# Performance work log

Measured on AMD Instinct MI355X. Metric: run time of the kernel, lower is better.

Reference implementation:

```python
import jax, jax.numpy as jnp
import numpy as np
from jax import lax

# Module config (from init_kwargs)
PADDING = (1, 1)
DILATION = (1, 1)
GROUPS = 1
# stride param is initialized to ones(2); effective integer stride = floor(stride) = (1, 1).
# Output shape depends on this value, so it must be static under jit.
INT_STRIDE = (1, 1)


def setup_inputs() -> dict:
    key = jax.random.key(0)
    k1, k2 = jax.random.split(key)
    B, Cin, H, W = 32, 128, 64, 64
    Cout, kH, kW = 256, 3, 3
    x = jax.random.normal(k1, (B, Cin, H, W), dtype=jnp.float32)
    # reset_parameters: uniform(-stdv, stdv), stdv = 1/sqrt(Cin*kH*kW)
    stdv = 1.0 / np.sqrt(Cin * kH * kW)
    weight = jax.random.uniform(k2, (Cout, Cin // GROUPS, kH, kW), dtype=jnp.float32,
                                minval=-stdv, maxval=stdv)
    stride = jnp.ones((2,), dtype=jnp.float32)
    return {"x": x, "weight": weight, "stride": stride}


def reference(x, weight, stride):
    # Integer strides = floor(stride); with stride initialized to ones this is (1, 1).
    # (Static under jit; floor has zero derivative a.e., so stride only affects
    #  sampling locations, exactly as in the CUDA im2col forward.)
    out = lax.conv_general_dilated(
        x, weight,
        window_strides=INT_STRIDE,
        padding=[(PADDING[0], PADDING[0]), (PADDING[1], PADDING[1])],
        rhs_dilation=DILATION,
        dimension_numbers=("NCHW", "OIHW", "NCHW"),
        feature_group_count=GROUPS,
    )
    return out
```

## Files before the change

### kernel.cpp

```cpp
#include <hip/hip_runtime.h>

typedef __attribute__((ext_vector_type(8))) short short8;
typedef __attribute__((ext_vector_type(4))) float f32x4;

#define XP_ELEMS (32u * 66u * 66u * 128u)
#define WT_ELEMS (256u * 1152u)
#define WS_NEED  ((size_t)(XP_ELEMS + WT_ELEMS) * 2u)

typedef const __attribute__((address_space(1))) void* gp1_t;
typedef __attribute__((address_space(3))) void* lp3_t;

__device__ __forceinline__ void gload16(const void* g, void* l) {
  __builtin_amdgcn_global_load_lds((gp1_t)g, (lp3_t)l, 16, 0, 0);
}

__device__ __forceinline__ short f2bf(float f) {
  unsigned u = __float_as_uint(f);
  u = (u + 0x7FFFu + ((u >> 16) & 1u)) >> 16;
  return (short)u;
}

__global__ __launch_bounds__(256) void prepass_x(const float* __restrict__ x,
                                                 short* __restrict__ xp) {
  __shared__ short lds[64 * 128];
  const int y = blockIdx.x;
  const int b = blockIdx.y;
  const int t = threadIdx.x;

  const float* src = x + (long)b * 128 * 4096 + y * 64;
#pragma unroll
  for (int i = 0; i < 8; ++i) {
    int f4 = t + i * 256;
    int cin = f4 >> 4, px4 = f4 & 15;
    float4 v = *(const float4*)(src + (long)cin * 4096 + px4 * 4);
    float vv[4] = {v.x, v.y, v.z, v.w};
#pragma unroll
    for (int j = 0; j < 4; ++j) {
      int px = px4 * 4 + j;
      int g = (cin >> 3) ^ ((px ^ (px >> 2)) & 15);
      lds[px * 128 + (g << 3) + (cin & 7)] = f2bf(vv[j]);
    }
  }
  __syncthreads();
  short* dst = xp + ((long)(b * 66 + y + 1) * 66 + 1) * 128;
#pragma unroll
  for (int i = 0; i < 4; ++i) {
    int f8 = t + i * 256;
    int px = f8 >> 4, c8 = f8 & 15;
    int g = c8 ^ ((px ^ (px >> 2)) & 15);
    short8 v = *(const short8*)&lds[px * 128 + (g << 3)];
    *(short8*)(dst + (long)px * 128 + c8 * 8) = v;
  }
  short8 z = (short8)0;
  short* rowbase = xp + (long)(b * 66 + y + 1) * 66 * 128;
  if (t < 32) {
    int px = (t < 16) ? 0 : 65;
    int c8 = t & 15;
    *(short8*)(rowbase + (long)px * 128 + c8 * 8) = z;
  }
  if (y == 0) {
    short* r0 = xp + (long)(b * 66) * 66 * 128;
    for (int idx = t; idx < 66 * 16; idx += 256) *(short8*)(r0 + idx * 8) = z;
  }
  if (y == 63) {
    short* r65 = xp + ((long)(b * 66) + 65) * 66 * 128;
    for (int idx = t; idx < 66 * 16; idx += 256) *(short8*)(r65 + idx * 8) = z;
  }
}

__global__ __launch_bounds__(256) void prepass_w(const float* __restrict__ w,
                                                 short* __restrict__ wt) {
  int o    = blockIdx.x * 256 + threadIdx.x;
  int cout = o / 1152;
  int r    = o % 1152;
  int kh   = r / 384;
  int kw   = (r / 128) % 3;
  int cin  = r & 127;
  wt[o] = f2bf(w[((cout * 128 + cin) * 3 + kh) * 3 + kw]);
}

__global__ __launch_bounds__(512, 2) void conv_gemm(const short* __restrict__ xp,
                                                    const short* __restrict__ wt,
                                                    float* __restrict__ out) {
  __shared__ alignas(16) short Alds[2 * 2 * 2 * 128 * 32];
  __shared__ alignas(16) short Blds[2 * 2 * 2 * 128 * 32];
  const int tid = threadIdx.x;
  const int w   = tid >> 6;
  const int l   = tid & 63;
  const int l15 = l & 15;
  const int q   = l >> 4;
  const int wm2 = w >> 2;
  const int wn4 = w & 3;
  const int ntile = blockIdx.x;

  const int r6 = (tid >> 2) & 63;
  const int cc = tid >> 8;
  const int pp = tid & 3;
  const int cs = pp ^ ((r6 >> 1) & 3);
  const int aTh  = r6 * 1152 + cc * 32 + cs * 8;
  const int ldsA = cc * 4096 + r6 * 32 + pp * 8;
  const int ldsB0 = ldsA + ((r6 & 32) << 5);
  int bTh[2][2];
#pragma unroll
  for (int hb = 0; hb < 2; ++hb)
#pragma unroll
    for (int nq = 0; nq < 2; ++nq) {
      int R  = (r6 & 31) + ((r6 >> 5) << 6) + nq * 32;
      int n  = (ntile << 8) + (hb << 7) + R;
      int bb = n >> 12, yy = (n >> 6) & 63, xx = n & 63;
      bTh[hb][nq] = ((bb * 66 + yy) * 66 + xx) * 128 + cc * 32 + cs * 8;
    }

  int aRd[8], bRd[4];
#pragma unroll
  for (int mi = 0; mi < 8; ++mi) {
    int r = (mi << 4) + l15;
    aRd[mi] = r * 32 + ((q ^ ((r >> 1) & 3)) << 3);
  }
#pragma unroll
  for (int nj = 0; nj < 4; ++nj) {
    int r = ((wn4 & 1) << 6) + (nj << 4) + l15;
    bRd[nj] = r * 32 + ((q ^ ((r >> 1) & 3)) << 3);
  }
  const int aHB = wm2 * 8192;
  const int bHB = (wn4 >> 1) * 8192;

  f32x4 acc[8][4];
#pragma unroll
  for (int mi = 0; mi < 8; ++mi)
#pragma unroll
    for (int nj = 0; nj < 4; ++nj) acc[mi][nj] = (f32x4)0.f;

  short8 af[4][2], bf[4][2];

  auto ST_A = [&](int s, int v, int kb) {
    gload16(wt + kb + v * 73728 + aTh,
            &Alds[s * 16384 + v * 2048 + ldsA]);
    gload16(wt + kb + 147456 + v * 73728 + aTh,
            &Alds[s * 16384 + 8192 + v * 2048 + ldsA]);
  };
  auto ST_B = [&](int s, int nq, int sh) {
    gload16(xp + sh + bTh[0][nq], &Blds[s * 16384 + (nq << 10) + ldsB0]);
    gload16(xp + sh + bTh[1][nq], &Blds[s * 16384 + 8192 + (nq << 10) + ldsB0]);
  };
  auto LD_A = [&](int s, int mq) {
#pragma unroll
    for (int i = 0; i < 4; ++i)
#pragma unroll
      for (int c = 0; c < 2; ++c)
        af[i][c] = *(const short8*)&Alds[s * 16384 + aHB + c * 4096 + aRd[mq * 4 + i]];
  };
  auto LD_B = [&](int s, int nq) {
#pragma unroll
    for (int j = 0; j < 2; ++j)
#pragma unroll
      for (int c = 0; c < 2; ++c)
        bf[nq * 2 + j][c] =
            *(const short8*)&Blds[s * 16384 + bHB + c * 4096 + bRd[nq * 2 + j]];
  };
  auto MM = [&](int mq, int nq) {
    __builtin_amdgcn_s_setprio(1);
#pragma unroll
    for (int c = 0; c < 2; ++c)
#pragma unroll
      for (int i = 0; i < 4; ++i)
#pragma unroll
        for (int j = 0; j < 2; ++j)
          acc[mq * 4 + i][nq * 2 + j] = __builtin_amdgcn_mfma_f32_16x16x32_bf16(
              af[i][c], bf[nq * 2 + j][c], acc[mq * 4 + i][nq * 2 + j], 0, 0, 0);
    __builtin_amdgcn_s_setprio(0);
  };

#define BAR()   do { __builtin_amdgcn_s_barrier(); \
                     asm volatile("" ::: "memory"); } while (0)
#define LGKM0() asm volatile("s_waitcnt lgkmcnt(0)" ::: "memory")
#define VMC(n)  asm volatile("s_waitcnt vmcnt(" #n ")" ::: "memory")

  ST_A(0, 0, 0);  ST_B(0, 0, 0);
  ST_A(0, 1, 0);  ST_B(0, 1, 0);
  ST_A(1, 0, 64); ST_B(1, 0, 64);
  VMC(4);
  BAR();

#pragma unroll
  for (int J = 0; J < 9; ++J) {
    const int kh  = J / 3,        kw  = J % 3;
    const int khn = (J + 1) / 3,  kwn = (J + 1) % 3;
    const int kb1 = J * 128 + 64;
    const int kb2 = (J + 1) * 128;
    const int sh1 = (kh * 66 + kw) * 128 + 64;
    const int sh2 = (khn * 66 + kwn) * 128;
    const int sh3 = sh2 + 64;

    LD_A(0, 0); LD_B(0, 0);
    ST_A(1, 1, kb1);
    LGKM0(); MM(0, 0);
    LD_B(0, 1);
    ST_B(1, 1, sh1);
    LGKM0(); MM(0, 1);
    BAR();

    LD_A(0, 1);
    if (J < 8) ST_A(0, 0, kb2);
    LGKM0(); MM(1, 0);
    if (J < 8) ST_B(0, 0, sh2);
    LGKM0(); MM(1, 1);
    if (J < 8) { VMC(4); } else { VMC(0); }
    BAR();

    LD_A(1, 0); LD_B(1, 0);
    if (J < 8) ST_A(0, 1, kb2);
    LGKM0(); MM(0, 0);
    LD_B(1, 1);
    if (J < 8) ST_B(0, 1, sh2);
    LGKM0(); MM(0, 1);
    BAR();

    LD_A(1, 1);
    if (J < 8) ST_A(1, 0, kb2 + 64);
    LGKM0(); MM(1, 0);
    if (J < 8) ST_B(1, 0, sh3);
    LGKM0(); MM(1, 1);
    if (J < 8) { VMC(4); BAR(); }
  }

  const int bimg = ntile >> 4;
  const int yx0  = ((ntile & 15) << 8) + (wn4 << 6) + l15;
  float* outb = out + (long)bimg * (256 * 4096) + yx0;
#pragma unroll
  for (int mi = 0; mi < 8; ++mi) {
#pragma unroll
    for (int r = 0; r < 4; ++r) {
      const int cout = (wm2 << 7) + (mi << 4) + (q << 2) + r;
      float* orow = outb + (long)cout * 4096;
#pragma unroll
      for (int nj = 0; nj < 4; ++nj) orow[nj << 4] = acc[mi][nj][r];
    }
  }
#undef BAR
#undef LGKM0
#undef VMC
}

__global__ __launch_bounds__(256) void naive_conv(const float* __restrict__ x,
                                                  const float* __restrict__ wgt,
                                                  float* __restrict__ out) {
  long o = (long)blockIdx.x * 256 + threadIdx.x;
  int xx = (int)(o & 63);
  int y  = (int)((o >> 6) & 63);
  int co = (int)((o >> 12) & 255);
  int b  = (int)(o >> 20);
  float s = 0.f;
  for (int ci = 0; ci < 128; ++ci) {
    for (int kh = 0; kh < 3; ++kh) {
      int iy = y + kh - 1;
      if (iy < 0 || iy > 63) continue;
      for (int kw = 0; kw < 3; ++kw) {
        int ix = xx + kw - 1;
        if (ix < 0 || ix > 63) continue;
        s += x[((long)(b * 128 + ci) * 64 + iy) * 64 + ix] *
             wgt[((co * 128 + ci) * 3 + kh) * 3 + kw];
      }
    }
  }
  out[o] = s;
}

extern "C" void kernel_launch(void* const* d_in, const int* in_sizes, int n_in,
                              void* d_out, int out_size, void* d_ws, size_t ws_size,
                              hipStream_t stream) {
  (void)in_sizes; (void)n_in;
  const float* x   = (const float*)d_in[0];
  const float* wgt = (const float*)d_in[1];
  float* out = (float*)d_out;
  if (ws_size >= WS_NEED) {
    short* xp = (short*)d_ws;
    short* wt = xp + XP_ELEMS;
    prepass_x<<<dim3(64, 32), dim3(256), 0, stream>>>(x, xp);
    prepass_w<<<dim3(WT_ELEMS / 256), dim3(256), 0, stream>>>(wgt, wt);
    conv_gemm<<<dim3(512), dim3(512), 0, stream>>>(xp, wt, out);
  } else {
    naive_conv<<<dim3(out_size / 256), dim3(256), 0, stream>>>(x, wgt, out);
  }
}
```

Before: 254.2 us.

## Load weights directly from global into MFMA fragments with pre-swizzled layout

```diff
diff --git a/kernel.cpp b/kernel.cpp
--- a/kernel.cpp
+++ b/kernel.cpp
@@ -9,6 +9,7 @@
 
 typedef const __attribute__((address_space(1))) void* gp1_t;
 typedef __attribute__((address_space(3))) void* lp3_t;
+typedef const __attribute__((address_space(1))) short8* g8p_t;
 
 __device__ __forceinline__ void gload16(const void* g, void* l) {
   __builtin_amdgcn_global_load_lds((gp1_t)g, (lp3_t)l, 16, 0, 0);
@@ -76,14 +77,16 @@
   int kh   = r / 384;
   int kw   = (r / 128) % 3;
   int cin  = r & 127;
-  wt[o] = f2bf(w[((cout * 128 + cin) * 3 + kh) * 3 + kw]);
+  int mb = cout >> 4, l15 = cout & 15;
+  int c32 = r >> 5, q = (r >> 3) & 3, k7 = r & 7;
+  wt[((mb * 36 + c32) << 9) + (l15 << 5) + (q << 3) + k7] =
+      f2bf(w[((cout * 128 + cin) * 3 + kh) * 3 + kw]);
 }
 
 __global__ __launch_bounds__(512, 2) void conv_gemm(const short* __restrict__ xp,
                                                     const short* __restrict__ wt,
                                                     float* __restrict__ out) {
-  __shared__ alignas(16) short Alds[2 * 2 * 2 * 128 * 32];
-  __shared__ alignas(16) short Blds[2 * 2 * 2 * 128 * 32];
+  __shared__ alignas(16) short Blds[2 * 16384];
   const int tid = threadIdx.x;
   const int w   = tid >> 6;
   const int l   = tid & 63;
@@ -97,9 +100,7 @@
   const int cc = tid >> 8;
   const int pp = tid & 3;
   const int cs = pp ^ ((r6 >> 1) & 3);
-  const int aTh  = r6 * 1152 + cc * 32 + cs * 8;
-  const int ldsA = cc * 4096 + r6 * 32 + pp * 8;
-  const int ldsB0 = ldsA + ((r6 & 32) << 5);
+  const int ldsB0 = cc * 4096 + r6 * 32 + pp * 8 + ((r6 & 32) << 5);
   int bTh[2][2];
 #pragma unroll
   for (int hb = 0; hb < 2; ++hb)
@@ -111,46 +112,49 @@
       bTh[hb][nq] = ((bb * 66 + yy) * 66 + xx) * 128 + cc * 32 + cs * 8;
     }
 
-  int aRd[8], bRd[4];
-#pragma unroll
-  for (int mi = 0; mi < 8; ++mi) {
-    int r = (mi << 4) + l15;
-    aRd[mi] = r * 32 + ((q ^ ((r >> 1) & 3)) << 3);
-  }
+  int bRd[4];
 #pragma unroll
   for (int nj = 0; nj < 4; ++nj) {
     int r = ((wn4 & 1) << 6) + (nj << 4) + l15;
     bRd[nj] = r * 32 + ((q ^ ((r >> 1) & 3)) << 3);
   }
-  const int aHB = wm2 * 8192;
   const int bHB = (wn4 >> 1) * 8192;
 
+  const int aV = l15 * 32 + q * 8;
+
   f32x4 acc[8][4];
 #pragma unroll
   for (int mi = 0; mi < 8; ++mi)
 #pragma unroll
     for (int nj = 0; nj < 4; ++nj) acc[mi][nj] = (f32x4)0.f;
 
-  short8 af[4][2], bf[4][2];
-
-  auto ST_A = [&](int s, int v, int kb) {
-    gload16(wt + kb + v * 73728 + aTh,
-            &Alds[s * 16384 + v * 2048 + ldsA]);
-    gload16(wt + kb + 147456 + v * 73728 + aTh,
-            &Alds[s * 16384 + 8192 + v * 2048 + ldsA]);
+  short8 afA[4][2], afB[4][2], bf[4][2];
+
+#define BAR()   do { __builtin_amdgcn_s_barrier(); \
+                     asm volatile("" ::: "memory"); } while (0)
+#define LGK0()  asm volatile("s_waitcnt lgkmcnt(0)" ::: "memory")
+#define VMC(n)  asm volatile("s_waitcnt vmcnt(" #n ")" ::: "memory")
+
+  auto ALOAD = [&](int T, int mq, short8 (&d)[4][2]) {
+    const int mb0 = wm2 * 8 + mq * 4;
+#pragma unroll
+    for (int i = 0; i < 4; ++i)
+#pragma unroll
+      for (int c = 0; c < 2; ++c)
+        d[i][c] = *(g8p_t)(wt + (((long)((mb0 + i) * 36 + 2 * T + c) << 9) + aV));
   };
   auto ST_B = [&](int s, int nq, int sh) {
     gload16(xp + sh + bTh[0][nq], &Blds[s * 16384 + (nq << 10) + ldsB0]);
     gload16(xp + sh + bTh[1][nq], &Blds[s * 16384 + 8192 + (nq << 10) + ldsB0]);
   };
-  auto LD_A = [&](int s, int mq) {
-#pragma unroll
-    for (int i = 0; i < 4; ++i)
-#pragma unroll
-      for (int c = 0; c < 2; ++c)
-        af[i][c] = *(const short8*)&Alds[s * 16384 + aHB + c * 4096 + aRd[mq * 4 + i]];
-  };
-  auto LD_B = [&](int s, int nq) {
+  auto BSTAGE = [&](int T) {
+    const int J = T >> 1, h = T & 1;
+    const int kh = J / 3, kw = J - kh * 3;
+    const int sh = (kh * 66 + kw) * 128 + h * 64;
+    ST_B(T & 1, 0, sh);
+    ST_B(T & 1, 1, sh);
+  };
+  auto BREAD = [&](int s, int nq) {
 #pragma unroll
     for (int j = 0; j < 2; ++j)
 #pragma unroll
@@ -158,7 +162,7 @@
         bf[nq * 2 + j][c] =
             *(const short8*)&Blds[s * 16384 + bHB + c * 4096 + bRd[nq * 2 + j]];
   };
-  auto MM = [&](int mq, int nq) {
+  auto MM = [&](short8 (&a)[4][2], int mq, int nq) {
     __builtin_amdgcn_s_setprio(1);
 #pragma unroll
     for (int c = 0; c < 2; ++c)
@@ -167,62 +171,42 @@
 #pragma unroll
         for (int j = 0; j < 2; ++j)
           acc[mq * 4 + i][nq * 2 + j] = __builtin_amdgcn_mfma_f32_16x16x32_bf16(
-              af[i][c], bf[nq * 2 + j][c], acc[mq * 4 + i][nq * 2 + j], 0, 0, 0);
+              a[i][c], bf[nq * 2 + j][c], acc[mq * 4 + i][nq * 2 + j], 0, 0, 0);
     __builtin_amdgcn_s_setprio(0);
   };
 
-#define BAR()   do { __builtin_amdgcn_s_barrier(); \
-                     asm volatile("" ::: "memory"); } while (0)
-#define LGKM0() asm volatile("s_waitcnt lgkmcnt(0)" ::: "memory")
-#define VMC(n)  asm volatile("s_waitcnt vmcnt(" #n ")" ::: "memory")
-
-  ST_A(0, 0, 0);  ST_B(0, 0, 0);
-  ST_A(0, 1, 0);  ST_B(0, 1, 0);
-  ST_A(1, 0, 64); ST_B(1, 0, 64);
-  VMC(4);
+  BSTAGE(0);
+  ALOAD(0, 0, afA);
+  VMC(8);
   BAR();
 
-#pragma unroll
-  for (int J = 0; J < 9; ++J) {
-    const int kh  = J / 3,        kw  = J % 3;
-    const int khn = (J + 1) / 3,  kwn = (J + 1) % 3;
-    const int kb1 = J * 128 + 64;
-    const int kb2 = (J + 1) * 128;
-    const int sh1 = (kh * 66 + kw) * 128 + 64;
-    const int sh2 = (khn * 66 + kwn) * 128;
-    const int sh3 = sh2 + 64;
-
-    LD_A(0, 0); LD_B(0, 0);
-    ST_A(1, 1, kb1);
-    LGKM0(); MM(0, 0);
-    LD_B(0, 1);
-    ST_B(1, 1, sh1);
-    LGKM0(); MM(0, 1);
+#pragma unroll 1
+  for (int T = 0; T < 17; ++T) {
+    const int s = T & 1;
+    ALOAD(T, 1, afB);
+    BREAD(s, 0);
+    LGK0();
+    MM(afA, 0, 0);
+    BREAD(s, 1);
+    BSTAGE(T + 1);
+    LGK0();
+    MM(afA, 0, 1);
+    ALOAD(T + 1, 0, afA);
+    MM(afB, 1, 0);
+    MM(afB, 1, 1);
+    VMC(8);
     BAR();
-
-    LD_A(0, 1);
-    if (J < 8) ST_A(0, 0, kb2);
-    LGKM0(); MM(1, 0);
-    if (J < 8) ST_B(0, 0, sh2);
-    LGKM0(); MM(1, 1);
-    if (J < 8) { VMC(4); } else { VMC(0); }
-    BAR();
-
-    LD_A(1, 0); LD_B(1, 0);
-    if (J < 8) ST_A(0, 1, kb2);
-    LGKM0(); MM(0, 0);
-    LD_B(1, 1);
-    if (J < 8) ST_B(0, 1, sh2);
-    LGKM0(); MM(0, 1);
-    BAR();
-
-    LD_A(1, 1);
-    if (J < 8) ST_A(1, 0, kb2 + 64);
-    LGKM0(); MM(1, 0);
-    if (J < 8) ST_B(1, 0, sh3);
-    LGKM0(); MM(1, 1);
-    if (J < 8) { VMC(4); BAR(); }
-  }
+  }
+
+  ALOAD(17, 1, afB);
+  BREAD(1, 0);
+  LGK0();
+  MM(afA, 0, 0);
+  BREAD(1, 1);
+  LGK0();
+  MM(afA, 0, 1);
+  MM(afB, 1, 0);
+  MM(afB, 1, 1);
 
   const int bimg = ntile >> 4;
   const int yx0  = ((ntile & 15) << 8) + (wn4 << 6) + l15;
@@ -238,7 +222,7 @@
     }
   }
 #undef BAR
-#undef LGKM0
+#undef LGK0
 #undef VMC
 }
 
```

Result: slower. 279.7 us (+10.0%).
